# Kernel optimization log

Hardware: AMD Instinct MI355X
Metric: run time of the kernel (lower is better)

The kernel has to match this reference:

```python
import jax, jax.numpy as jnp
import numpy as np

S, B, IN, H, OUT = 128, 256, 1024, 1024, 1024

def setup_inputs() -> dict:
    key = jax.random.key(0)
    ks = jax.random.split(key, 10)
    sc_ih = 1.0 / np.sqrt(IN)
    sc_h = 1.0 / np.sqrt(H)
    return {
        "inputs": jax.random.normal(ks[0], (S, B, IN), dtype=jnp.float32),
        "h0": jax.random.normal(ks[1], (B, H), dtype=jnp.float32),
        "c0": jax.random.normal(ks[2], (B, H), dtype=jnp.float32),
        "W_ih": jax.random.normal(ks[3], (4 * H, IN), dtype=jnp.float32) * sc_ih,
        "W_hh": jax.random.normal(ks[4], (4 * H, H), dtype=jnp.float32) * sc_h,
        "b_ih": jax.random.normal(ks[5], (4 * H,), dtype=jnp.float32) * sc_h,
        "b_hh": jax.random.normal(ks[6], (4 * H,), dtype=jnp.float32) * sc_h,
        "attnW": jax.random.normal(ks[7], (S, S), dtype=jnp.float32),
        "linW": jax.random.normal(ks[8], (OUT, H), dtype=jnp.float32) * sc_h,
        "linb": jax.random.normal(ks[9], (OUT,), dtype=jnp.float32) * sc_h,
    }

def _lstm_scan(inputs, h0, c0, W_ih, W_hh, b_ih, b_hh):
    # PyTorch LSTM gate order: i, f, g, o
    def step(carry, x_t):
        h, c = carry
        gates = x_t @ W_ih.T + b_ih + h @ W_hh.T + b_hh  # [B, 4H]
        i, f, g, o = jnp.split(gates, 4, axis=-1)
        i = jax.nn.sigmoid(i)
        f = jax.nn.sigmoid(f)
        g = jnp.tanh(g)
        o = jax.nn.sigmoid(o)
        c = f * c + i * g
        h = o * jnp.tanh(c)
        return (h, c), h
    (_, _), hs = jax.lax.scan(step, (h0, c0), inputs)
    return hs  # [S, B, H]

def reference(inputs, h0, c0, W_ih, W_hh, b_ih, b_hh, attnW, linW, linb):
    hs = _lstm_scan(inputs, h0, c0, W_ih, W_hh, b_ih, b_hh)  # [S, B, H]
    A = jax.nn.softmax(attnW, axis=-1)  # F.softmax default on 2D -> dim=1
    att = jnp.einsum('xy,ybh->xbh', A, hs)  # weighted sum of hidden states
    out = att @ linW.T + linb  # [S, B, OUT]
    return out.reshape(-1, OUT)  # [S*B, OUT]
```

## Files before the change

### kernel.cpp

```cpp
#include <hip/hip_runtime.h>


typedef _Float16 half8 __attribute__((ext_vector_type(8)));
typedef float f32x4 __attribute__((ext_vector_type(4)));

#define S_  128
#define B_  256
#define HDIM 1024
#define BH  262144
#define K2  2048

__device__ __forceinline__ void g2l16(void* lds_base, const void* g) {
  __builtin_amdgcn_global_load_lds(
      (const __attribute__((address_space(1))) void*)g,
      (__attribute__((address_space(3))) void*)lds_base, 16, 0, 0);
}

__device__ __forceinline__ float sigmoidf_(float x) {
  return 1.f / (1.f + __expf(-x));
}
__device__ __forceinline__ float tanhf_(float x) {
  float e = __expf(-2.f * fabsf(x));
  float t = (1.f - e) / (1.f + e);
  return x < 0.f ? -t : t;
}

__global__ __launch_bounds__(256) void k_cvt(const float* __restrict__ src,
                                             _Float16* __restrict__ dst) {
  size_t i = ((size_t)blockIdx.x * 256 + threadIdx.x) * 8;
  float4 u = *(const float4*)(src + i);
  float4 v = *(const float4*)(src + i + 4);
  half8 h;
  h[0] = u.x; h[1] = u.y; h[2] = u.z; h[3] = u.w;
  h[4] = v.x; h[5] = v.y; h[6] = v.z; h[7] = v.w;
  *(half8*)(dst + i) = h;
}

__global__ __launch_bounds__(256) void k_wcat(const float* __restrict__ Wih,
                                              const float* __restrict__ Whh,
                                              _Float16* __restrict__ Wc) {
  size_t i = ((size_t)blockIdx.x * 256 + threadIdx.x) * 8;
  int r = (int)(i >> 11), k = (int)(i & 2047);
  const float* src = (k < 1024) ? (Wih + (size_t)r * 1024 + k)
                                : (Whh + (size_t)r * 1024 + (k - 1024));
  float4 u = *(const float4*)(src);
  float4 v = *(const float4*)(src + 4);
  half8 h;
  h[0] = u.x; h[1] = u.y; h[2] = u.z; h[3] = u.w;
  h[4] = v.x; h[5] = v.y; h[6] = v.z; h[7] = v.w;
  *(half8*)(Wc + i) = h;
}

__global__ __launch_bounds__(256) void k_init(const float* __restrict__ h0,
                                              const float* __restrict__ c0,
                                              const float* __restrict__ bih,
                                              const float* __restrict__ bhh,
                                              _Float16* __restrict__ hs0,
                                              float* __restrict__ cbuf,
                                              float* __restrict__ bias) {
  int i = blockIdx.x * 256 + threadIdx.x;
  cbuf[i] = c0[i];
  hs0[i] = (_Float16)h0[i];
  if (i < 4096) bias[i] = bih[i] + bhh[i];
}

__global__ __launch_bounds__(64) void k_softmax(const float* __restrict__ W,
                                                _Float16* __restrict__ Ah,
                                                _Float16* __restrict__ Ar) {
  int r = blockIdx.x, lane = threadIdx.x;
  float v0 = W[r * 128 + lane], v1 = W[r * 128 + 64 + lane];
  float m = fmaxf(v0, v1);
  for (int off = 32; off; off >>= 1) m = fmaxf(m, __shfl_xor(m, off));
  float e0 = __expf(v0 - m), e1 = __expf(v1 - m);
  float s = e0 + e1;
  for (int off = 32; off; off >>= 1) s += __shfl_xor(s, off);
  float inv = 1.f / s;
  float a0 = e0 * inv, a1 = e1 * inv;
  _Float16 h0 = (_Float16)a0, h1 = (_Float16)a1;
  Ah[r * 128 + lane] = h0;
  Ah[r * 128 + 64 + lane] = h1;
  Ar[r * 128 + lane] = (_Float16)(a0 - (float)h0);
  Ar[r * 128 + 64 + lane] = (_Float16)(a1 - (float)h1);
}

__global__ __launch_bounds__(256) void k_step(const _Float16* __restrict__ Xh,
                                              const _Float16* __restrict__ Wc,
                                              const float* __restrict__ bias,
                                              _Float16* __restrict__ hs,
                                              float* __restrict__ cbuf,
                                              int t) {
  __shared__ char smem[65536];
  const int tid = threadIdx.x;
  const int wave = tid >> 6;
  const int lane = tid & 63;
  const int n_tile = blockIdx.x & 63;
  const int m_tile = blockIdx.x >> 6;
  const int n0 = n_tile * 16;
  const int m0 = m_tile * 64;

  const _Float16* Xt = Xh + (size_t)t * BH;
  const _Float16* Hp = hs + (size_t)t * BH;

  f32x4 acc[4];
  #pragma unroll
  for (int g = 0; g < 4; ++g) acc[g] = (f32x4){0.f, 0.f, 0.f, 0.f};

  int offA[2], offB[2];
  #pragma unroll
  for (int q = 0; q < 4; ++q) {
    int s = q * 256 + tid;
    if (q < 2) {
      int r = s >> 3, c = s & 7;
      int kc = c ^ (r & 7);
      offA[q] = (m0 + r) * 1024 + kc * 8;
    } else {
      int sb = s - 512;
      int r = sb >> 3, c = sb & 7;
      int kc = c ^ (r & 7);
      int row = (r >> 4) * 1024 + n0 + (r & 15);
      offB[q - 2] = row * 2048 + kc * 8;
    }
  }

  auto stage = [&](int buf, int k0) {
    char* base = smem + buf * 16384;
    const _Float16* Ab = (k0 < 1024) ? (Xt + k0) : (Hp + (k0 - 1024));
    #pragma unroll
    for (int q = 0; q < 4; ++q) {
      char* dst = base + (q * 4 + wave) * 1024;
      if (q < 2) g2l16(dst, Ab + offA[q]);
      else       g2l16(dst, Wc + offB[q - 2] + k0);
    }
  };

  const int ra = wave * 16 + (lane & 15);
  const int kcl = lane >> 4;
  const int aoff0 = ra * 128 + ((kcl ^ (ra & 7)) * 16);
  const int aoff1 = ra * 128 + (((kcl + 4) ^ (ra & 7)) * 16);
  int boff0[4], boff1[4];
  #pragma unroll
  for (int g = 0; g < 4; ++g) {
    int rb = g * 16 + (lane & 15);
    boff0[g] = 8192 + rb * 128 + ((kcl ^ (rb & 7)) * 16);
    boff1[g] = 8192 + rb * 128 + (((kcl + 4) ^ (rb & 7)) * 16);
  }

  stage(0, 0);
  stage(1, 64);
  stage(2, 128);

  #pragma unroll
  for (int iter = 0; iter < 32; ++iter) {
    if (iter < 29) stage((iter + 3) & 3, (iter + 3) * 64);
    if (iter < 29)       asm volatile("s_waitcnt vmcnt(12)" ::: "memory");
    else if (iter == 29) asm volatile("s_waitcnt vmcnt(8)"  ::: "memory");
    else if (iter == 30) asm volatile("s_waitcnt vmcnt(4)"  ::: "memory");
    else                 asm volatile("s_waitcnt vmcnt(0)"  ::: "memory");
    __builtin_amdgcn_s_barrier();
    const char* At = smem + (iter & 3) * 16384;
    half8 a0 = *(const half8*)(At + aoff0);
    half8 a1 = *(const half8*)(At + aoff1);
    #pragma unroll
    for (int g = 0; g < 4; ++g) {
      half8 b0 = *(const half8*)(At + boff0[g]);
      acc[g] = __builtin_amdgcn_mfma_f32_16x16x32_f16(a0, b0, acc[g], 0, 0, 0);
    }
    #pragma unroll
    for (int g = 0; g < 4; ++g) {
      half8 b1 = *(const half8*)(At + boff1[g]);
      acc[g] = __builtin_amdgcn_mfma_f32_16x16x32_f16(a1, b1, acc[g], 0, 0, 0);
    }
    __builtin_amdgcn_s_barrier();
  }

  int n = n0 + (lane & 15);
  float bi = bias[n], bf = bias[1024 + n], bg = bias[2048 + n], bo = bias[3072 + n];
  int mrow0 = m0 + wave * 16 + (lane >> 4) * 4;
  _Float16* hnext = hs + (size_t)(t + 1) * BH;
  #pragma unroll
  for (int r = 0; r < 4; ++r) {
    size_t idx = (size_t)(mrow0 + r) * 1024 + n;
    float gi = sigmoidf_(acc[0][r] + bi);
    float gf = sigmoidf_(acc[1][r] + bf);
    float gg = tanhf_(acc[2][r] + bg);
    float go = sigmoidf_(acc[3][r] + bo);
    float c = gf * cbuf[idx] + gi * gg;
    cbuf[idx] = c;
    hnext[idx] = (_Float16)(go * tanhf_(c));
  }
}

__global__ __launch_bounds__(256) void k_attn(const _Float16* __restrict__ Ah,
                                              const _Float16* __restrict__ Ar,
                                              const _Float16* __restrict__ hs,
                                              _Float16* __restrict__ att) {
  __shared__ char smem[131072];
  const int tid = threadIdx.x;
  const int wave = tid >> 6;
  const int lane = tid & 63;
  const int n0 = blockIdx.x * 256;

  #pragma unroll
  for (int q = 0; q < 16; ++q) {
    int s = q * 256 + tid;
    char* dst = smem + (q * 4 + wave) * 1024;
    if (q < 8) {
      int r = s >> 4;
      int cl = (s & 15) ^ (r & 15);
      g2l16(dst, Ah + r * 128 + cl * 8);
    } else {
      int s2 = s - 2048;
      int r = s2 >> 4;
      int cl = (s2 & 15) ^ (r & 15);
      g2l16(dst, Ar + r * 128 + cl * 8);
    }
  }
  #pragma unroll
  for (int ch = 0; ch < 4; ++ch) {
    char* base = smem + 65536 + ch * 16384;
    #pragma unroll
    for (int q = 0; q < 4; ++q) {
      int s = q * 256 + tid;
      int y = s >> 5, cp = s & 31;
      int cl = cp ^ (((y >> 3) & 3) << 1);
      g2l16(base + (q * 4 + wave) * 1024,
            hs + (size_t)(1 + ch * 32 + y) * BH + n0 + cl * 8);
    }
  }

  f32x4 acc[8][4];
  #pragma unroll
  for (int m = 0; m < 8; ++m)
    #pragma unroll
    for (int nf = 0; nf < 4; ++nf) acc[m][nf] = (f32x4){0.f, 0.f, 0.f, 0.f};

  const int yg = lane >> 4;

  #pragma unroll
  for (int ch = 0; ch < 4; ++ch) {
    if (ch == 0)      asm volatile("s_waitcnt vmcnt(12)" ::: "memory");
    else if (ch == 1) asm volatile("s_waitcnt vmcnt(8)"  ::: "memory");
    else if (ch == 2) asm volatile("s_waitcnt vmcnt(4)"  ::: "memory");
    else              asm volatile("s_waitcnt vmcnt(0)"  ::: "memory");
    __builtin_amdgcn_s_barrier();

    const char* cb = smem + 65536 + ch * 16384;
    half8 b[4];
    #pragma unroll
    for (int nf = 0; nf < 4; ++nf) {
      int n = wave * 64 + nf * 16 + (lane & 15);
      const char* col = cb + (((n >> 3) ^ (yg << 1)) * 16) + (n & 7) * 2;
      #pragma unroll
      for (int j = 0; j < 8; ++j)
        b[nf][j] = *(const _Float16*)(col + (yg * 8 + j) * 512);
    }
    #pragma unroll
    for (int m = 0; m < 8; ++m) {
      int x = m * 16 + (lane & 15);
      int sw = ((ch * 4 + yg) ^ (x & 15)) * 16;
      half8 ah = *(const half8*)(smem + x * 256 + sw);
      half8 ar = *(const half8*)(smem + 32768 + x * 256 + sw);
      #pragma unroll
      for (int nf = 0; nf < 4; ++nf) {
        acc[m][nf] = __builtin_amdgcn_mfma_f32_16x16x32_f16(ah, b[nf], acc[m][nf], 0, 0, 0);
        acc[m][nf] = __builtin_amdgcn_mfma_f32_16x16x32_f16(ar, b[nf], acc[m][nf], 0, 0, 0);
      }
    }
  }

  #pragma unroll
  for (int m = 0; m < 8; ++m) {
    int x0 = m * 16 + (lane >> 4) * 4;
    #pragma unroll
    for (int nf = 0; nf < 4; ++nf) {
      int n = n0 + wave * 64 + nf * 16 + (lane & 15);
      #pragma unroll
      for (int r = 0; r < 4; ++r)
        att[(size_t)(x0 + r) * BH + n] = (_Float16)acc[m][nf][r];
    }
  }
}

__global__ __launch_bounds__(256) void k_final(const _Float16* __restrict__ att,
                                               const _Float16* __restrict__ Wl,
                                               const float* __restrict__ bvec,
                                               float* __restrict__ out) {
  __shared__ char smem[65536];
  const int tid = threadIdx.x, wave = tid >> 6, lane = tid & 63;
  const int m0 = (blockIdx.x >> 3) * 128;
  const int n0 = (blockIdx.x & 7) * 128;
  const int mh = (wave & 1) * 64, nh = (wave >> 1) * 64;

  f32x4 acc[4][4];
  #pragma unroll
  for (int i = 0; i < 4; ++i)
    #pragma unroll
    for (int j = 0; j < 4; ++j) acc[i][j] = (f32x4){0.f, 0.f, 0.f, 0.f};

  auto stage = [&](int p, int k0) {
    char* base = smem + p * 32768;
    #pragma unroll
    for (int q = 0; q < 8; ++q) {
      int grp = q * 4 + wave;
      char* dst = base + grp * 1024;
      int s = grp * 64 + lane;
      if (s < 1024) {
        int r = s >> 3, c = s & 7;
        int kc = c ^ (r & 7);
        g2l16(dst, att + (size_t)(m0 + r) * 1024 + k0 + kc * 8);
      } else {
        int sb = s - 1024;
        int r = sb >> 3, c = sb & 7;
        int kc = c ^ (r & 7);
        g2l16(dst, Wl + (size_t)(n0 + r) * 1024 + k0 + kc * 8);
      }
    }
  };

  stage(0, 0);
  for (int iter = 0; iter < 16; ++iter) {
    int p = iter & 1;
    __syncthreads();
    if (iter + 1 < 16) stage(1 - p, (iter + 1) * 64);
    const char* At = smem + p * 32768;
    const char* Bt = At + 16384;
    #pragma unroll
    for (int k32 = 0; k32 < 2; ++k32) {
      int kc = k32 * 4 + (lane >> 4);
      half8 a[4], b[4];
      #pragma unroll
      for (int i = 0; i < 4; ++i) {
        int ra = mh + i * 16 + (lane & 15);
        a[i] = *(const half8*)(At + ra * 128 + ((kc ^ (ra & 7)) * 16));
        int rb = nh + i * 16 + (lane & 15);
        b[i] = *(const half8*)(Bt + rb * 128 + ((kc ^ (rb & 7)) * 16));
      }
      #pragma unroll
      for (int i = 0; i < 4; ++i)
        #pragma unroll
        for (int j = 0; j < 4; ++j)
          acc[i][j] = __builtin_amdgcn_mfma_f32_16x16x32_f16(a[i], b[j], acc[i][j], 0, 0, 0);
    }
  }

  #pragma unroll
  for (int i = 0; i < 4; ++i) {
    int m = m0 + mh + i * 16 + (lane >> 4) * 4;
    #pragma unroll
    for (int j = 0; j < 4; ++j) {
      int n = n0 + nh + j * 16 + (lane & 15);
      float bv = bvec[n];
      #pragma unroll
      for (int r = 0; r < 4; ++r)
        out[(size_t)(m + r) * 1024 + n] = acc[i][j][r] + bv;
    }
  }
}

extern "C" void kernel_launch(void* const* d_in, const int* in_sizes, int n_in,
                              void* d_out, int out_size, void* d_ws, size_t ws_size,
                              hipStream_t stream) {
  const float* X     = (const float*)d_in[0];
  const float* h0    = (const float*)d_in[1];
  const float* c0    = (const float*)d_in[2];
  const float* Wih   = (const float*)d_in[3];
  const float* Whh   = (const float*)d_in[4];
  const float* bih   = (const float*)d_in[5];
  const float* bhh   = (const float*)d_in[6];
  const float* attnW = (const float*)d_in[7];
  const float* linW  = (const float*)d_in[8];
  const float* linb  = (const float*)d_in[9];
  float* out = (float*)d_out;
  char* ws = (char*)d_ws;

  _Float16* Xh  = (_Float16*)(ws + 0);
  _Float16* Wc  = (_Float16*)(ws + 67108864);
  _Float16* Wl  = (_Float16*)(ws + 83886080);
  _Float16* hs  = (_Float16*)(ws + 85983232);
  _Float16* att = (_Float16*)(ws + 153616384);
  float* cbuf   = (float*)(ws + 220725248);
  float* bias   = (float*)(ws + 221773824);
  _Float16* Ahm = (_Float16*)(ws + 221790208);
  _Float16* Arm = (_Float16*)(ws + 221822976);

  k_cvt<<<16384, 256, 0, stream>>>(X, Xh);
  k_wcat<<<4096, 256, 0, stream>>>(Wih, Whh, Wc);
  k_cvt<<<512, 256, 0, stream>>>(linW, Wl);
  k_init<<<1024, 256, 0, stream>>>(h0, c0, bih, bhh, hs, cbuf, bias);
  k_softmax<<<128, 64, 0, stream>>>(attnW, Ahm, Arm);

  for (int t = 0; t < S_; ++t)
    k_step<<<256, 256, 0, stream>>>(Xh, Wc, bias, hs, cbuf, t);

  k_attn<<<1024, 256, 0, stream>>>(Ahm, Arm, hs, att);
  k_final<<<2048, 256, 0, stream>>>(att, Wl, linb, out);
}
```

Before: 1.729 ms.

## Hoist input projection out of recurrence into chunked batched GEMMs

Splits the LSTM gate GEMM: the x_t·W_ih term for 16 timesteps at a time is computed by a large tiled GEMM (k_gx) into an fp32 gate buffer with the summed bias, and the per-step kernel now only does the h·W_hh half (K=1024 instead of 2048) and adds the precomputed gates. This halves the serial per-step work on the critical path, at the cost of extra fp32 global traffic for the gate buffer, which reuses the att workspace region. It also drops the trailing barrier in the step loop, shortens the prefetch depth, and remaps block indices in k_gx/k_final so tiles are grouped per XCD.

Result: slower. 1.772 ms (+2.5%).

```diff
diff --git a/kernel.cpp b/kernel.cpp
--- a/kernel.cpp
+++ b/kernel.cpp
@@ -8,7 +8,6 @@
 #define B_  256
 #define HDIM 1024
 #define BH  262144
-#define K2  2048
 
 __device__ __forceinline__ void g2l16(void* lds_base, const void* g) {
   __builtin_amdgcn_global_load_lds(
@@ -34,21 +33,6 @@
   h[0] = u.x; h[1] = u.y; h[2] = u.z; h[3] = u.w;
   h[4] = v.x; h[5] = v.y; h[6] = v.z; h[7] = v.w;
   *(half8*)(dst + i) = h;
-}
-
-__global__ __launch_bounds__(256) void k_wcat(const float* __restrict__ Wih,
-                                              const float* __restrict__ Whh,
-                                              _Float16* __restrict__ Wc) {
-  size_t i = ((size_t)blockIdx.x * 256 + threadIdx.x) * 8;
-  int r = (int)(i >> 11), k = (int)(i & 2047);
-  const float* src = (k < 1024) ? (Wih + (size_t)r * 1024 + k)
-                                : (Whh + (size_t)r * 1024 + (k - 1024));
-  float4 u = *(const float4*)(src);
-  float4 v = *(const float4*)(src + 4);
-  half8 h;
-  h[0] = u.x; h[1] = u.y; h[2] = u.z; h[3] = u.w;
-  h[4] = v.x; h[5] = v.y; h[6] = v.z; h[7] = v.w;
-  *(half8*)(Wc + i) = h;
 }
 
 __global__ __launch_bounds__(256) void k_init(const float* __restrict__ h0,
@@ -83,9 +67,85 @@
   Ar[r * 128 + 64 + lane] = (_Float16)(a1 - (float)h1);
 }
 
-__global__ __launch_bounds__(256) void k_step(const _Float16* __restrict__ Xh,
-                                              const _Float16* __restrict__ Wc,
-                                              const float* __restrict__ bias,
+__global__ __launch_bounds__(256) void k_gx(const _Float16* __restrict__ Xc,
+                                            const _Float16* __restrict__ Wi,
+                                            const float* __restrict__ bvec,
+                                            float* __restrict__ Gx) {
+  __shared__ char smem[65536];
+  const int tid = threadIdx.x, wave = tid >> 6, lane = tid & 63;
+  const int j = blockIdx.x >> 3, xcd = blockIdx.x & 7;
+  const int m0 = (xcd * 4 + ((j >> 3) & 3)) * 128;
+  const int n0 = ((j & 7) | ((j >> 5) << 3)) * 128;
+  const int mh = (wave & 1) * 64, nh = (wave >> 1) * 64;
+
+  f32x4 acc[4][4];
+  #pragma unroll
+  for (int i = 0; i < 4; ++i)
+    #pragma unroll
+    for (int jj = 0; jj < 4; ++jj) acc[i][jj] = (f32x4){0.f, 0.f, 0.f, 0.f};
+
+  auto stage = [&](int p, int k0) {
+    char* base = smem + p * 32768;
+    #pragma unroll
+    for (int q = 0; q < 8; ++q) {
+      int grp = q * 4 + wave;
+      char* dst = base + grp * 1024;
+      int s = grp * 64 + lane;
+      if (s < 1024) {
+        int r = s >> 3, c = s & 7;
+        int kc = c ^ (r & 7);
+        g2l16(dst, Xc + (size_t)(m0 + r) * 1024 + k0 + kc * 8);
+      } else {
+        int sb = s - 1024;
+        int r = sb >> 3, c = sb & 7;
+        int kc = c ^ (r & 7);
+        g2l16(dst, Wi + (size_t)(n0 + r) * 1024 + k0 + kc * 8);
+      }
+    }
+  };
+
+  stage(0, 0);
+  for (int iter = 0; iter < 16; ++iter) {
+    int p = iter & 1;
+    __syncthreads();
+    if (iter + 1 < 16) stage(1 - p, (iter + 1) * 64);
+    const char* At = smem + p * 32768;
+    const char* Bt = At + 16384;
+    #pragma unroll
+    for (int k32 = 0; k32 < 2; ++k32) {
+      int kc = k32 * 4 + (lane >> 4);
+      half8 a[4], b[4];
+      #pragma unroll
+      for (int i = 0; i < 4; ++i) {
+        int ra = mh + i * 16 + (lane & 15);
+        a[i] = *(const half8*)(At + ra * 128 + ((kc ^ (ra & 7)) * 16));
+        int rb = nh + i * 16 + (lane & 15);
+        b[i] = *(const half8*)(Bt + rb * 128 + ((kc ^ (rb & 7)) * 16));
+      }
+      #pragma unroll
+      for (int i = 0; i < 4; ++i)
+        #pragma unroll
+        for (int jj = 0; jj < 4; ++jj)
+          acc[i][jj] = __builtin_amdgcn_mfma_f32_16x16x32_f16(a[i], b[jj], acc[i][jj], 0, 0, 0);
+    }
+  }
+
+  #pragma unroll
+  for (int i = 0; i < 4; ++i) {
+    int m = m0 + mh + i * 16 + (lane >> 4) * 4;
+    #pragma unroll
+    for (int jj = 0; jj < 4; ++jj) {
+      int n = n0 + nh + jj * 16 + (lane & 15);
+      float bv = bvec[n];
+      #pragma unroll
+      for (int r = 0; r < 4; ++r)
+        Gx[(size_t)(m + r) * 4096 + n] = acc[i][jj][r] + bv;
+    }
+  }
+}
+
+__global__ __launch_bounds__(256) void k_step(const float* __restrict__ Gx,
+                                              const _Float16* __restrict__ Wh,
                                               _Float16* __restrict__ hs,
                                               float* __restrict__ cbuf,
                                               int t) {
@@ -98,7 +158,6 @@
   const int n0 = n_tile * 16;
   const int m0 = m_tile * 64;
 
-  const _Float16* Xt = Xh + (size_t)t * BH;
   const _Float16* Hp = hs + (size_t)t * BH;
 
   f32x4 acc[4];
@@ -118,18 +177,17 @@
       int r = sb >> 3, c = sb & 7;
       int kc = c ^ (r & 7);
       int row = (r >> 4) * 1024 + n0 + (r & 15);
-      offB[q - 2] = row * 2048 + kc * 8;
+      offB[q - 2] = row * 1024 + kc * 8;
     }
   }
 
   auto stage = [&](int buf, int k0) {
     char* base = smem + buf * 16384;
-    const _Float16* Ab = (k0 < 1024) ? (Xt + k0) : (Hp + (k0 - 1024));
     #pragma unroll
     for (int q = 0; q < 4; ++q) {
       char* dst = base + (q * 4 + wave) * 1024;
-      if (q < 2) g2l16(dst, Ab + offA[q]);
-      else       g2l16(dst, Wc + offB[q - 2] + k0);
+      if (q < 2) g2l16(dst, Hp + offA[q] + k0);
+      else       g2l16(dst, Wh + offB[q - 2] + k0);
     }
   };
 
@@ -147,15 +205,13 @@
 
   stage(0, 0);
   stage(1, 64);
-  stage(2, 128);
-
-  #pragma unroll
-  for (int iter = 0; iter < 32; ++iter) {
-    if (iter < 29) stage((iter + 3) & 3, (iter + 3) * 64);
-    if (iter < 29)       asm volatile("s_waitcnt vmcnt(12)" ::: "memory");
-    else if (iter == 29) asm volatile("s_waitcnt vmcnt(8)"  ::: "memory");
-    else if (iter == 30) asm volatile("s_waitcnt vmcnt(4)"  ::: "memory");
-    else                 asm volatile("s_waitcnt vmcnt(0)"  ::: "memory");
+
+  #pragma unroll
+  for (int iter = 0; iter < 16; ++iter) {
+    if (iter < 14) stage((iter + 2) & 3, (iter + 2) * 64);
+    if (iter < 14)       asm volatile("s_waitcnt vmcnt(8)" ::: "memory");
+    else if (iter == 14) asm volatile("s_waitcnt vmcnt(4)" ::: "memory");
+    else                 asm volatile("s_waitcnt vmcnt(0)" ::: "memory");
     __builtin_amdgcn_s_barrier();
     const char* At = smem + (iter & 3) * 16384;
     half8 a0 = *(const half8*)(At + aoff0);
@@ -170,20 +226,20 @@
       half8 b1 = *(const half8*)(At + boff1[g]);
       acc[g] = __builtin_amdgcn_mfma_f32_16x16x32_f16(a1, b1, acc[g], 0, 0, 0);
     }
-    __builtin_amdgcn_s_barrier();
   }
 
   int n = n0 + (lane & 15);
-  float bi = bias[n], bf = bias[1024 + n], bg = bias[2048 + n], bo = bias[3072 + n];
   int mrow0 = m0 + wave * 16 + (lane >> 4) * 4;
+  const float* gx = Gx + (size_t)(t & 15) * 1048576;
   _Float16* hnext = hs + (size_t)(t + 1) * BH;
   #pragma unroll
   for (int r = 0; r < 4; ++r) {
+    size_t gidx = (size_t)(mrow0 + r) * 4096 + n;
+    float gi = sigmoidf_(acc[0][r] + gx[gidx]);
+    float gf = sigmoidf_(acc[1][r] + gx[gidx + 1024]);
+    float gg = tanhf_(acc[2][r] + gx[gidx + 2048]);
+    float go = sigmoidf_(acc[3][r] + gx[gidx + 3072]);
     size_t idx = (size_t)(mrow0 + r) * 1024 + n;
-    float gi = sigmoidf_(acc[0][r] + bi);
-    float gf = sigmoidf_(acc[1][r] + bf);
-    float gg = tanhf_(acc[2][r] + bg);
-    float go = sigmoidf_(acc[3][r] + bo);
     float c = gf * cbuf[idx] + gi * gg;
     cbuf[idx] = c;
     hnext[idx] = (_Float16)(go * tanhf_(c));
@@ -287,15 +343,16 @@
                                                float* __restrict__ out) {
   __shared__ char smem[65536];
   const int tid = threadIdx.x, wave = tid >> 6, lane = tid & 63;
-  const int m0 = (blockIdx.x >> 3) * 128;
-  const int n0 = (blockIdx.x & 7) * 128;
+  const int j = blockIdx.x >> 3;
+  const int m0 = (((blockIdx.x & 7) << 5) | (j >> 3)) * 128;
+  const int n0 = (j & 7) * 128;
   const int mh = (wave & 1) * 64, nh = (wave >> 1) * 64;
 
   f32x4 acc[4][4];
   #pragma unroll
   for (int i = 0; i < 4; ++i)
     #pragma unroll
-    for (int j = 0; j < 4; ++j) acc[i][j] = (f32x4){0.f, 0.f, 0.f, 0.f};
+    for (int jj = 0; jj < 4; ++jj) acc[i][jj] = (f32x4){0.f, 0.f, 0.f, 0.f};
 
   auto stage = [&](int p, int k0) {
     char* base = smem + p * 32768;
@@ -338,8 +395,8 @@
       #pragma unroll
       for (int i = 0; i < 4; ++i)
         #pragma unroll
-        for (int j = 0; j < 4; ++j)
-          acc[i][j] = __builtin_amdgcn_mfma_f32_16x16x32_f16(a[i], b[j], acc[i][j], 0, 0, 0);
+        for (int jj = 0; jj < 4; ++jj)
+          acc[i][jj] = __builtin_amdgcn_mfma_f32_16x16x32_f16(a[i], b[jj], acc[i][jj], 0, 0, 0);
     }
   }
 
@@ -347,12 +404,12 @@
   for (int i = 0; i < 4; ++i) {
     int m = m0 + mh + i * 16 + (lane >> 4) * 4;
     #pragma unroll
-    for (int j = 0; j < 4; ++j) {
-      int n = n0 + nh + j * 16 + (lane & 15);
+    for (int jj = 0; jj < 4; ++jj) {
+      int n = n0 + nh + jj * 16 + (lane & 15);
       float bv = bvec[n];
       #pragma unroll
       for (int r = 0; r < 4; ++r)
-        out[(size_t)(m + r) * 1024 + n] = acc[i][j][r] + bv;
+        out[(size_t)(m + r) * 1024 + n] = acc[i][jj][r] + bv;
     }
   }
 }
@@ -374,23 +431,32 @@
   char* ws = (char*)d_ws;
 
   _Float16* Xh  = (_Float16*)(ws + 0);
-  _Float16* Wc  = (_Float16*)(ws + 67108864);
+  _Float16* Wi  = (_Float16*)(ws + 67108864);
+  _Float16* Wh  = (_Float16*)(ws + 75497472);
   _Float16* Wl  = (_Float16*)(ws + 83886080);
   _Float16* hs  = (_Float16*)(ws + 85983232);
-  _Float16* att = (_Float16*)(ws + 153616384);
+  char*     GxA = (ws + 153616384);
+  float*    GxF = (float*)GxA;
+  _Float16* att = (_Float16*)GxA;
   float* cbuf   = (float*)(ws + 220725248);
   float* bias   = (float*)(ws + 221773824);
   _Float16* Ahm = (_Float16*)(ws + 221790208);
   _Float16* Arm = (_Float16*)(ws + 221822976);
 
   k_cvt<<<16384, 256, 0, stream>>>(X, Xh);
-  k_wcat<<<4096, 256, 0, stream>>>(Wih, Whh, Wc);
+  k_cvt<<<2048, 256, 0, stream>>>(Wih, Wi);
+  k_cvt<<<2048, 256, 0, stream>>>(Whh, Wh);
   k_cvt<<<512, 256, 0, stream>>>(linW, Wl);
   k_init<<<1024, 256, 0, stream>>>(h0, c0, bih, bhh, hs, cbuf, bias);
   k_softmax<<<128, 64, 0, stream>>>(attnW, Ahm, Arm);
 
-  for (int t = 0; t < S_; ++t)
-    k_step<<<256, 256, 0, stream>>>(Xh, Wc, bias, hs, cbuf, t);
+  for (int g = 0; g < 8; ++g) {
+    k_gx<<<1024, 256, 0, stream>>>(Xh + (size_t)g * 4096 * 1024, Wi, bias, GxF);
+    for (int tl = 0; tl < 16; ++tl) {
+      int t = g * 16 + tl;
+      k_step<<<256, 256, 0, stream>>>(GxF, Wh, hs, cbuf, t);
+    }
+  }
 
   k_attn<<<1024, 256, 0, stream>>>(Ahm, Arm, hs, att);
   k_final<<<2048, 256, 0, stream>>>(att, Wl, linb, out);
```

## Restructure LSTM step GEMM with 32x32 MFMA, split-K waves, direct A loads

Applied to the files above, without the earlier changes.

The per-timestep gate GEMM now uses 32x32x16 MFMAs, with waves split two ways over M and two ways over K. A fragments are loaded straight from global memory into registers two iterations ahead, so only the W tile is staged in LDS. Partial sums from the two K halves are reduced through LDS before the elementwise LSTM update. The final linear kernel also remaps block indices so blocks sharing weight columns are spread across XCDs/L2. The goal is fewer MFMA instructions and less LDS traffic per step, at the cost of an extra LDS reduction and sync.

Result: slower. 2.763 ms (+59.8%).

```diff
diff --git a/kernel.cpp b/kernel.cpp
--- a/kernel.cpp
+++ b/kernel.cpp
@@ -3,12 +3,12 @@
 
 typedef _Float16 half8 __attribute__((ext_vector_type(8)));
 typedef float f32x4 __attribute__((ext_vector_type(4)));
+typedef float f32x16 __attribute__((ext_vector_type(16)));
 
 #define S_  128
 #define B_  256
 #define HDIM 1024
 #define BH  262144
-#define K2  2048
 
 __device__ __forceinline__ void g2l16(void* lds_base, const void* g) {
   __builtin_amdgcn_global_load_lds(
@@ -91,8 +91,10 @@
                                               int t) {
   __shared__ char smem[65536];
   const int tid = threadIdx.x;
-  const int wave = tid >> 6;
+  const int wid = tid >> 6;
   const int lane = tid & 63;
+  const int mh = wid & 1;
+  const int kh = wid >> 1;
   const int n_tile = blockIdx.x & 63;
   const int m_tile = blockIdx.x >> 6;
   const int n0 = n_tile * 16;
@@ -101,92 +103,133 @@
   const _Float16* Xt = Xh + (size_t)t * BH;
   const _Float16* Hp = hs + (size_t)t * BH;
 
-  f32x4 acc[4];
-  #pragma unroll
-  for (int g = 0; g < 4; ++g) acc[g] = (f32x4){0.f, 0.f, 0.f, 0.f};
-
-  int offA[2], offB[2];
-  #pragma unroll
-  for (int q = 0; q < 4; ++q) {
+  f32x16 acc0 = {0.f};
+  f32x16 acc1 = {0.f};
+
+  int offB[2];
+  #pragma unroll
+  for (int q = 0; q < 2; ++q) {
     int s = q * 256 + tid;
-    if (q < 2) {
-      int r = s >> 3, c = s & 7;
-      int kc = c ^ (r & 7);
-      offA[q] = (m0 + r) * 1024 + kc * 8;
-    } else {
-      int sb = s - 512;
-      int r = sb >> 3, c = sb & 7;
-      int kc = c ^ (r & 7);
-      int row = (r >> 4) * 1024 + n0 + (r & 15);
-      offB[q - 2] = row * 2048 + kc * 8;
-    }
-  }
-
+    int r = s >> 3, c = s & 7;
+    int kc = (c - r) & 7;
+    offB[q] = ((r >> 4) * 1024 + n0 + (r & 15)) * 2048 + kc * 8;
+  }
   auto stage = [&](int buf, int k0) {
-    char* base = smem + buf * 16384;
-    const _Float16* Ab = (k0 < 1024) ? (Xt + k0) : (Hp + (k0 - 1024));
-    #pragma unroll
-    for (int q = 0; q < 4; ++q) {
-      char* dst = base + (q * 4 + wave) * 1024;
-      if (q < 2) g2l16(dst, Ab + offA[q]);
-      else       g2l16(dst, Wc + offB[q - 2] + k0);
-    }
+    char* base = smem + buf * 8192;
+    #pragma unroll
+    for (int q = 0; q < 2; ++q)
+      g2l16(base + (q * 4 + wid) * 1024, Wc + offB[q] + k0);
   };
 
-  const int ra = wave * 16 + (lane & 15);
-  const int kcl = lane >> 4;
-  const int aoff0 = ra * 128 + ((kcl ^ (ra & 7)) * 16);
-  const int aoff1 = ra * 128 + (((kcl + 4) ^ (ra & 7)) * 16);
-  int boff0[4], boff1[4];
-  #pragma unroll
-  for (int g = 0; g < 4; ++g) {
-    int rb = g * 16 + (lane & 15);
-    boff0[g] = 8192 + rb * 128 + ((kcl ^ (rb & 7)) * 16);
-    boff1[g] = 8192 + rb * 128 + (((kcl + 4) ^ (rb & 7)) * 16);
-  }
-
+  const int arow = m0 + mh * 32 + (lane & 31);
+  const int acol = kh * 32 + (lane >> 5) * 8;
+  auto loadA = [&](int i, half8& a0, half8& a1) {
+    int k = i * 64 + acol;
+    const _Float16* src = (i < 16) ? (Xt + (size_t)arow * 1024 + k)
+                                   : (Hp + (size_t)arow * 1024 + (k - 1024));
+    a0 = *(const half8*)(src);
+    a1 = *(const half8*)(src + 16);
+  };
+
+  auto rdB = [&](const char* bb, int f, int j) -> half8 {
+    int r = f * 32 + (lane & 31);
+    int cd = 4 * kh + 2 * j + (lane >> 5);
+    return *(const half8*)(bb + r * 128 + (((cd + r) & 7) * 16));
+  };
+
+  half8 a00, a01, a10, a11;
+  loadA(0, a00, a01);
+  loadA(1, a10, a11);
+  asm volatile("" ::: "memory");
   stage(0, 0);
+  asm volatile("" ::: "memory");
   stage(1, 64);
+  asm volatile("" ::: "memory");
   stage(2, 128);
-
-  #pragma unroll
-  for (int iter = 0; iter < 32; ++iter) {
-    if (iter < 29) stage((iter + 3) & 3, (iter + 3) * 64);
-    if (iter < 29)       asm volatile("s_waitcnt vmcnt(12)" ::: "memory");
-    else if (iter == 29) asm volatile("s_waitcnt vmcnt(8)"  ::: "memory");
-    else if (iter == 30) asm volatile("s_waitcnt vmcnt(4)"  ::: "memory");
-    else                 asm volatile("s_waitcnt vmcnt(0)"  ::: "memory");
+  asm volatile("" ::: "memory");
+
+  #pragma unroll
+  for (int i = 0; i < 32; ++i) {
+    const int vn = (i == 0) ? 4 : (i == 1) ? 6 : (i <= 29) ? 8
+                 : (i == 30) ? 6 : 2;
+    if (vn == 4)      asm volatile("s_waitcnt vmcnt(4)" ::: "memory");
+    else if (vn == 6) asm volatile("s_waitcnt vmcnt(6)" ::: "memory");
+    else if (vn == 8) asm volatile("s_waitcnt vmcnt(8)" ::: "memory");
+    else              asm volatile("s_waitcnt vmcnt(2)" ::: "memory");
     __builtin_amdgcn_s_barrier();
-    const char* At = smem + (iter & 3) * 16384;
-    half8 a0 = *(const half8*)(At + aoff0);
-    half8 a1 = *(const half8*)(At + aoff1);
-    #pragma unroll
-    for (int g = 0; g < 4; ++g) {
-      half8 b0 = *(const half8*)(At + boff0[g]);
-      acc[g] = __builtin_amdgcn_mfma_f32_16x16x32_f16(a0, b0, acc[g], 0, 0, 0);
-    }
-    #pragma unroll
-    for (int g = 0; g < 4; ++g) {
-      half8 b1 = *(const half8*)(At + boff1[g]);
-      acc[g] = __builtin_amdgcn_mfma_f32_16x16x32_f16(a1, b1, acc[g], 0, 0, 0);
-    }
-    __builtin_amdgcn_s_barrier();
-  }
-
-  int n = n0 + (lane & 15);
-  float bi = bias[n], bf = bias[1024 + n], bg = bias[2048 + n], bo = bias[3072 + n];
-  int mrow0 = m0 + wave * 16 + (lane >> 4) * 4;
-  _Float16* hnext = hs + (size_t)(t + 1) * BH;
-  #pragma unroll
-  for (int r = 0; r < 4; ++r) {
-    size_t idx = (size_t)(mrow0 + r) * 1024 + n;
-    float gi = sigmoidf_(acc[0][r] + bi);
-    float gf = sigmoidf_(acc[1][r] + bf);
-    float gg = tanhf_(acc[2][r] + bg);
-    float go = sigmoidf_(acc[3][r] + bo);
-    float c = gf * cbuf[idx] + gi * gg;
-    cbuf[idx] = c;
-    hnext[idx] = (_Float16)(go * tanhf_(c));
+
+    const char* bb = smem + (i & 3) * 8192;
+    half8 b00 = rdB(bb, 0, 0);
+    half8 b10 = rdB(bb, 1, 0);
+    half8 b01 = rdB(bb, 0, 1);
+    half8 b11 = rdB(bb, 1, 1);
+    acc0 = __builtin_amdgcn_mfma_f32_32x32x16_f16(a00, b00, acc0, 0, 0, 0);
+    acc1 = __builtin_amdgcn_mfma_f32_32x32x16_f16(a00, b10, acc1, 0, 0, 0);
+    acc0 = __builtin_amdgcn_mfma_f32_32x32x16_f16(a01, b01, acc0, 0, 0, 0);
+    acc1 = __builtin_amdgcn_mfma_f32_32x32x16_f16(a01, b11, acc1, 0, 0, 0);
+    a00 = a10; a01 = a11;
+
+    asm volatile("" ::: "memory");
+    if (i + 2 < 32) loadA(i + 2, a10, a11);
+    asm volatile("" ::: "memory");
+    if (i + 3 < 32) stage((i + 3) & 3, (i + 3) * 64);
+    asm volatile("" ::: "memory");
+  }
+
+  asm volatile("s_waitcnt vmcnt(0)" ::: "memory");
+  __syncthreads();
+
+  float* EX = (float*)(smem + 32768);
+  if (kh == 1) {
+    float* base = EX + mh * 2112;
+    #pragma unroll
+    for (int f = 0; f < 2; ++f) {
+      const f32x16 a = f ? acc1 : acc0;
+      int gr = f * 32 + (lane & 31);
+      #pragma unroll
+      for (int e = 0; e < 16; ++e) {
+        int mr = (e & 3) + 8 * (e >> 2) + 4 * (lane >> 5);
+        base[gr * 33 + mr] = a[e];
+      }
+    }
+  }
+  __syncthreads();
+  float* G = (float*)smem;
+  if (kh == 0) {
+    const float* base = EX + mh * 2112;
+    #pragma unroll
+    for (int f = 0; f < 2; ++f) {
+      const f32x16 a = f ? acc1 : acc0;
+      int gr = f * 32 + (lane & 31);
+      #pragma unroll
+      for (int e = 0; e < 16; ++e) {
+        int mr = (e & 3) + 8 * (e >> 2) + 4 * (lane >> 5);
+        G[(mh * 32 + mr) * 66 + gr] = a[e] + base[gr * 33 + mr];
+      }
+    }
+  }
+  __syncthreads();
+
+  {
+    int nl = tid & 15;
+    int mseg = tid >> 4;
+    int n = n0 + nl;
+    float bi = bias[n], bf2 = bias[1024 + n];
+    float bg = bias[2048 + n], bo = bias[3072 + n];
+    _Float16* hnext = hs + (size_t)(t + 1) * BH;
+    #pragma unroll
+    for (int rr = 0; rr < 4; ++rr) {
+      int m = mseg * 4 + rr;
+      const float* g = G + m * 66;
+      float gi = sigmoidf_(g[nl] + bi);
+      float gf = sigmoidf_(g[16 + nl] + bf2);
+      float gg = tanhf_(g[32 + nl] + bg);
+      float go = sigmoidf_(g[48 + nl] + bo);
+      size_t idx = (size_t)(m0 + m) * 1024 + n;
+      float c = gf * cbuf[idx] + gi * gg;
+      cbuf[idx] = c;
+      hnext[idx] = (_Float16)(go * tanhf_(c));
+    }
   }
 }
 
@@ -287,15 +330,16 @@
                                                float* __restrict__ out) {
   __shared__ char smem[65536];
   const int tid = threadIdx.x, wave = tid >> 6, lane = tid & 63;
-  const int m0 = (blockIdx.x >> 3) * 128;
-  const int n0 = (blockIdx.x & 7) * 128;
+  const int j = blockIdx.x >> 3;
+  const int m0 = (((blockIdx.x & 7) << 5) | (j >> 3)) * 128;
+  const int n0 = (j & 7) * 128;
   const int mh = (wave & 1) * 64, nh = (wave >> 1) * 64;
 
   f32x4 acc[4][4];
   #pragma unroll
   for (int i = 0; i < 4; ++i)
     #pragma unroll
-    for (int j = 0; j < 4; ++j) acc[i][j] = (f32x4){0.f, 0.f, 0.f, 0.f};
+    for (int jj = 0; jj < 4; ++jj) acc[i][jj] = (f32x4){0.f, 0.f, 0.f, 0.f};
 
   auto stage = [&](int p, int k0) {
     char* base = smem + p * 32768;
@@ -338,8 +382,8 @@
       #pragma unroll
       for (int i = 0; i < 4; ++i)
         #pragma unroll
-        for (int j = 0; j < 4; ++j)
-          acc[i][j] = __builtin_amdgcn_mfma_f32_16x16x32_f16(a[i], b[j], acc[i][j], 0, 0, 0);
+        for (int jj = 0; jj < 4; ++jj)
+          acc[i][jj] = __builtin_amdgcn_mfma_f32_16x16x32_f16(a[i], b[jj], acc[i][jj], 0, 0, 0);
     }
   }
 
@@ -347,12 +391,12 @@
   for (int i = 0; i < 4; ++i) {
     int m = m0 + mh + i * 16 + (lane >> 4) * 4;
     #pragma unroll
-    for (int j = 0; j < 4; ++j) {
-      int n = n0 + nh + j * 16 + (lane & 15);
+    for (int jj = 0; jj < 4; ++jj) {
+      int n = n0 + nh + jj * 16 + (lane & 15);
       float bv = bvec[n];
       #pragma unroll
       for (int r = 0; r < 4; ++r)
-        out[(size_t)(m + r) * 1024 + n] = acc[i][j][r] + bv;
+        out[(size_t)(m + r) * 1024 + n] = acc[i][jj][r] + bv;
     }
   }
 }
```

## Split LSTM step K dimension across two wave groups with LDS reduction

Applied to the files above, without the earlier changes.

Each k_step block now runs 512 threads. Two groups of four waves each handle half of the K=2048 reduction: one group takes the input projection and the other the recurrent projection. Partial accumulators are combined through LDS before the gate nonlinearities, and the pipeline now runs 16 iterations at prefetch depth 2. The aim is to halve the serial K loop per block in the latency-bound recurrent step, at the cost of doubling LDS to 128KB and adding an extra sync and reduction. The final GEMM's block-index mapping is also swizzled to improve L2 reuse.

Result: faster. 1.636 ms (-5.4%).

```diff
diff --git a/kernel.cpp b/kernel.cpp
--- a/kernel.cpp
+++ b/kernel.cpp
@@ -8,7 +8,6 @@
 #define B_  256
 #define HDIM 1024
 #define BH  262144
-#define K2  2048
 
 __device__ __forceinline__ void g2l16(void* lds_base, const void* g) {
   __builtin_amdgcn_global_load_lds(
@@ -83,23 +82,27 @@
   Ar[r * 128 + 64 + lane] = (_Float16)(a1 - (float)h1);
 }
 
-__global__ __launch_bounds__(256) void k_step(const _Float16* __restrict__ Xh,
+__global__ __launch_bounds__(512) void k_step(const _Float16* __restrict__ Xh,
                                               const _Float16* __restrict__ Wc,
                                               const float* __restrict__ bias,
                                               _Float16* __restrict__ hs,
                                               float* __restrict__ cbuf,
                                               int t) {
-  __shared__ char smem[65536];
+  __shared__ char smem[131072];
   const int tid = threadIdx.x;
-  const int wave = tid >> 6;
+  const int wid = tid >> 6;
   const int lane = tid & 63;
+  const int kg = wid >> 2;
+  const int wv = wid & 3;
+  const int tg = tid & 255;
   const int n_tile = blockIdx.x & 63;
   const int m_tile = blockIdx.x >> 6;
   const int n0 = n_tile * 16;
   const int m0 = m_tile * 64;
 
-  const _Float16* Xt = Xh + (size_t)t * BH;
-  const _Float16* Hp = hs + (size_t)t * BH;
+  const _Float16* Asrc = (kg == 0) ? (Xh + (size_t)t * BH)
+                                   : (hs + (size_t)t * BH);
+  const int kbase = kg * 1024;
 
   f32x4 acc[4];
   #pragma unroll
@@ -108,7 +111,7 @@
   int offA[2], offB[2];
   #pragma unroll
   for (int q = 0; q < 4; ++q) {
-    int s = q * 256 + tid;
+    int s = q * 256 + tg;
     if (q < 2) {
       int r = s >> 3, c = s & 7;
       int kc = c ^ (r & 7);
@@ -118,22 +121,22 @@
       int r = sb >> 3, c = sb & 7;
       int kc = c ^ (r & 7);
       int row = (r >> 4) * 1024 + n0 + (r & 15);
-      offB[q - 2] = row * 2048 + kc * 8;
-    }
-  }
-
+      offB[q - 2] = row * 2048 + kbase + kc * 8;
+    }
+  }
+
+  char* gbase = smem + kg * 65536;
   auto stage = [&](int buf, int k0) {
-    char* base = smem + buf * 16384;
-    const _Float16* Ab = (k0 < 1024) ? (Xt + k0) : (Hp + (k0 - 1024));
+    char* base = gbase + buf * 16384;
     #pragma unroll
     for (int q = 0; q < 4; ++q) {
-      char* dst = base + (q * 4 + wave) * 1024;
-      if (q < 2) g2l16(dst, Ab + offA[q]);
+      char* dst = base + (q * 4 + wv) * 1024;
+      if (q < 2) g2l16(dst, Asrc + offA[q] + k0);
       else       g2l16(dst, Wc + offB[q - 2] + k0);
     }
   };
 
-  const int ra = wave * 16 + (lane & 15);
+  const int ra = wv * 16 + (lane & 15);
   const int kcl = lane >> 4;
   const int aoff0 = ra * 128 + ((kcl ^ (ra & 7)) * 16);
   const int aoff1 = ra * 128 + (((kcl + 4) ^ (ra & 7)) * 16);
@@ -147,17 +150,15 @@
 
   stage(0, 0);
   stage(1, 64);
-  stage(2, 128);
-
-  #pragma unroll
-  for (int iter = 0; iter < 32; ++iter) {
-    if (iter < 29) stage((iter + 3) & 3, (iter + 3) * 64);
-    if (iter < 29)       asm volatile("s_waitcnt vmcnt(12)" ::: "memory");
-    else if (iter == 29) asm volatile("s_waitcnt vmcnt(8)"  ::: "memory");
-    else if (iter == 30) asm volatile("s_waitcnt vmcnt(4)"  ::: "memory");
-    else                 asm volatile("s_waitcnt vmcnt(0)"  ::: "memory");
+
+  #pragma unroll
+  for (int iter = 0; iter < 16; ++iter) {
+    if (iter < 14) stage((iter + 2) & 3, (iter + 2) * 64);
+    if (iter < 14)       asm volatile("s_waitcnt vmcnt(8)" ::: "memory");
+    else if (iter == 14) asm volatile("s_waitcnt vmcnt(4)" ::: "memory");
+    else                 asm volatile("s_waitcnt vmcnt(0)" ::: "memory");
     __builtin_amdgcn_s_barrier();
-    const char* At = smem + (iter & 3) * 16384;
+    const char* At = gbase + (iter & 3) * 16384;
     half8 a0 = *(const half8*)(At + aoff0);
     half8 a1 = *(const half8*)(At + aoff1);
     #pragma unroll
@@ -170,23 +171,46 @@
       half8 b1 = *(const half8*)(At + boff1[g]);
       acc[g] = __builtin_amdgcn_mfma_f32_16x16x32_f16(a1, b1, acc[g], 0, 0, 0);
     }
-    __builtin_amdgcn_s_barrier();
-  }
-
-  int n = n0 + (lane & 15);
-  float bi = bias[n], bf = bias[1024 + n], bg = bias[2048 + n], bo = bias[3072 + n];
-  int mrow0 = m0 + wave * 16 + (lane >> 4) * 4;
-  _Float16* hnext = hs + (size_t)(t + 1) * BH;
-  #pragma unroll
-  for (int r = 0; r < 4; ++r) {
-    size_t idx = (size_t)(mrow0 + r) * 1024 + n;
-    float gi = sigmoidf_(acc[0][r] + bi);
-    float gf = sigmoidf_(acc[1][r] + bf);
-    float gg = tanhf_(acc[2][r] + bg);
-    float go = sigmoidf_(acc[3][r] + bo);
-    float c = gf * cbuf[idx] + gi * gg;
-    cbuf[idx] = c;
-    hnext[idx] = (_Float16)(go * tanhf_(c));
+  }
+
+  __syncthreads();
+
+  {
+    float* EXg = (float*)smem + kg * 4224;
+    #pragma unroll
+    for (int g = 0; g < 4; ++g) {
+      int gc = g * 16 + (lane & 15);
+      int mb = wv * 16 + (lane >> 4) * 4;
+      #pragma unroll
+      for (int r = 0; r < 4; ++r)
+        EXg[(mb + r) * 66 + gc] = acc[g][r];
+    }
+  }
+  __syncthreads();
+
+  {
+    int nl = tid & 15;
+    int mseg = tid >> 4;
+    int n = n0 + nl;
+    float bi = bias[n], bf2 = bias[1024 + n];
+    float bg = bias[2048 + n], bo = bias[3072 + n];
+    const float* E0 = (float*)smem;
+    const float* E1 = E0 + 4224;
+    _Float16* hnext = hs + (size_t)(t + 1) * BH;
+    #pragma unroll
+    for (int rr = 0; rr < 2; ++rr) {
+      int m = mseg * 2 + rr;
+      const float* e0 = E0 + m * 66;
+      const float* e1 = E1 + m * 66;
+      float gi = sigmoidf_(e0[nl]      + e1[nl]      + bi);
+      float gf = sigmoidf_(e0[16 + nl] + e1[16 + nl] + bf2);
+      float gg = tanhf_   (e0[32 + nl] + e1[32 + nl] + bg);
+      float go = sigmoidf_(e0[48 + nl] + e1[48 + nl] + bo);
+      size_t idx = (size_t)(m0 + m) * 1024 + n;
+      float c = gf * cbuf[idx] + gi * gg;
+      cbuf[idx] = c;
+      hnext[idx] = (_Float16)(go * tanhf_(c));
+    }
   }
 }
 
@@ -287,15 +311,16 @@
                                                float* __restrict__ out) {
   __shared__ char smem[65536];
   const int tid = threadIdx.x, wave = tid >> 6, lane = tid & 63;
-  const int m0 = (blockIdx.x >> 3) * 128;
-  const int n0 = (blockIdx.x & 7) * 128;
+  const int j = blockIdx.x >> 3;
+  const int m0 = (((blockIdx.x & 7) << 5) | (j >> 3)) * 128;
+  const int n0 = (j & 7) * 128;
   const int mh = (wave & 1) * 64, nh = (wave >> 1) * 64;
 
   f32x4 acc[4][4];
   #pragma unroll
   for (int i = 0; i < 4; ++i)
     #pragma unroll
-    for (int j = 0; j < 4; ++j) acc[i][j] = (f32x4){0.f, 0.f, 0.f, 0.f};
+    for (int jj = 0; jj < 4; ++jj) acc[i][jj] = (f32x4){0.f, 0.f, 0.f, 0.f};
 
   auto stage = [&](int p, int k0) {
     char* base = smem + p * 32768;
@@ -338,8 +363,8 @@
       #pragma unroll
       for (int i = 0; i < 4; ++i)
         #pragma unroll
-        for (int j = 0; j < 4; ++j)
-          acc[i][j] = __builtin_amdgcn_mfma_f32_16x16x32_f16(a[i], b[j], acc[i][j], 0, 0, 0);
+        for (int jj = 0; jj < 4; ++jj)
+          acc[i][jj] = __builtin_amdgcn_mfma_f32_16x16x32_f16(a[i], b[jj], acc[i][jj], 0, 0, 0);
     }
   }
 
@@ -347,12 +372,12 @@
   for (int i = 0; i < 4; ++i) {
     int m = m0 + mh + i * 16 + (lane >> 4) * 4;
     #pragma unroll
-    for (int j = 0; j < 4; ++j) {
-      int n = n0 + nh + j * 16 + (lane & 15);
+    for (int jj = 0; jj < 4; ++jj) {
+      int n = n0 + nh + jj * 16 + (lane & 15);
       float bv = bvec[n];
       #pragma unroll
       for (int r = 0; r < 4; ++r)
-        out[(size_t)(m + r) * 1024 + n] = acc[i][j][r] + bv;
+        out[(size_t)(m + r) * 1024 + n] = acc[i][jj][r] + bv;
     }
   }
 }
@@ -390,7 +415,7 @@
   k_softmax<<<128, 64, 0, stream>>>(attnW, Ahm, Arm);
 
   for (int t = 0; t < S_; ++t)
-    k_step<<<256, 256, 0, stream>>>(Xh, Wc, bias, hs, cbuf, t);
+    k_step<<<256, 512, 0, stream>>>(Xh, Wc, bias, hs, cbuf, t);
 
   k_attn<<<1024, 256, 0, stream>>>(Ahm, Arm, hs, att);
   k_final<<<2048, 256, 0, stream>>>(att, Wl, linb, out);
```
